# Performance work log

Hardware: AMD Instinct MI355X
Metric: run time of the kernel (lower is better)

The kernel has to match this reference:

```python
import jax, jax.numpy as jnp
import numpy as np

B, T_TEXT, T_MEL = 8, 256, 1024
VOCAB, MEL, H = 256, 80, 512
NH, HD = 8, 64  # MultiheadAttention: 8 heads, head_dim 64


def _linear(x, w, b):
    return x @ w.T + b


def _lstm(x, w_ih, w_hh, b_ih, b_hh, reverse=False):
    # torch LSTM, gate order i,f,g,o; x: [B,T,Din] -> [B,T,H]
    xg = jnp.einsum('bti,gi->btg', x, w_ih) + b_ih  # precompute input contributions
    h0 = jnp.zeros((x.shape[0], w_hh.shape[1]), x.dtype)

    def step(carry, xt):
        h, c = carry
        g = xt + h @ w_hh.T + b_hh
        i, f, gg, o = jnp.split(g, 4, axis=-1)
        c = jax.nn.sigmoid(f) * c + jax.nn.sigmoid(i) * jnp.tanh(gg)
        h = jax.nn.sigmoid(o) * jnp.tanh(c)
        return (h, c), h

    _, hs = jax.lax.scan(step, (h0, h0), jnp.swapaxes(xg, 0, 1), reverse=reverse)
    return jnp.swapaxes(hs, 0, 1)


def _length_regulate(enc, durations, max_len):
    # Vectorized equivalent of the nested python loop: token j owns output
    # positions [cum[j-1], cum[j]); padded positions are zero, mask True=pad.
    dur = jnp.round(durations).astype(jnp.int32)
    cum = jnp.cumsum(dur, axis=1)                              # [B,T_text]
    pos = jnp.arange(max_len)                                  # [max_len]
    idx = jax.vmap(lambda c: jnp.searchsorted(c, pos, side='right'))(cum)
    pad_mask = pos[None, :] >= cum[:, -1:]                     # True = padded
    idx = jnp.minimum(idx, enc.shape[1] - 1)
    exp = jnp.take_along_axis(enc, idx[..., None], axis=1)     # [B,max_len,H]
    exp = exp * (~pad_mask)[..., None].astype(enc.dtype)
    return exp, pad_mask


def setup_inputs() -> dict:
    key = jax.random.key(0)
    ks = jax.random.split(key, 40)

    def rn(k, shape, scale=0.02):
        return jax.random.normal(k, shape, jnp.float32) * scale

    inp = {}
    inp['phoneme_indices'] = jax.random.randint(ks[0], (B, T_TEXT), 0, VOCAB)
    inp['mel_specs'] = jax.random.normal(ks[1], (B, T_MEL, MEL), jnp.float32)
    inp['phoneme_durations'] = jax.random.randint(ks[2], (B, T_TEXT), 0, 8).astype(jnp.float32)
    # parameters
    inp['emb'] = rn(ks[3], (VOCAB, H), 1.0)
    inp['enc_w_ih_f'] = rn(ks[4], (4 * H, H))
    inp['enc_w_hh_f'] = rn(ks[5], (4 * H, H))
    inp['enc_b_ih_f'] = rn(ks[6], (4 * H,))
    inp['enc_b_hh_f'] = rn(ks[7], (4 * H,))
    inp['enc_w_ih_b'] = rn(ks[8], (4 * H, H))
    inp['enc_w_hh_b'] = rn(ks[9], (4 * H, H))
    inp['enc_b_ih_b'] = rn(ks[10], (4 * H,))
    inp['enc_b_hh_b'] = rn(ks[11], (4 * H,))
    inp['proj_w'] = rn(ks[12], (H, 2 * H))
    inp['proj_b'] = rn(ks[13], (H,))
    inp['dur_w1'] = rn(ks[14], (H, H))
    inp['dur_b1'] = rn(ks[15], (H,))
    inp['dur_w2'] = rn(ks[16], (H // 2, H))
    inp['dur_b2'] = rn(ks[17], (H // 2,))
    inp['dur_w3'] = rn(ks[18], (1, H // 2))
    inp['dur_b3'] = rn(ks[19], (1,))
    inp['mel_in_w'] = rn(ks[20], (H, MEL))
    inp['mel_in_b'] = rn(ks[21], (H,))
    inp['attn_in_w'] = rn(ks[22], (3 * H, H))
    inp['attn_in_b'] = rn(ks[23], (3 * H,))
    inp['attn_out_w'] = rn(ks[24], (H, H))
    inp['attn_out_b'] = rn(ks[25], (H,))
    inp['dec_w_ih'] = rn(ks[26], (4 * H, 2 * H))
    inp['dec_w_hh'] = rn(ks[27], (4 * H, H))
    inp['dec_b_ih'] = rn(ks[28], (4 * H,))
    inp['dec_b_hh'] = rn(ks[29], (4 * H,))
    inp['mel_out_w'] = rn(ks[30], (MEL, H))
    inp['mel_out_b'] = rn(ks[31], (MEL,))
    return inp


def reference(phoneme_indices, mel_specs, phoneme_durations, emb,
              enc_w_ih_f, enc_w_hh_f, enc_b_ih_f, enc_b_hh_f,
              enc_w_ih_b, enc_w_hh_b, enc_b_ih_b, enc_b_hh_b,
              proj_w, proj_b, dur_w1, dur_b1, dur_w2, dur_b2, dur_w3, dur_b3,
              mel_in_w, mel_in_b, attn_in_w, attn_in_b, attn_out_w, attn_out_b,
              dec_w_ih, dec_w_hh, dec_b_ih, dec_b_hh, mel_out_w, mel_out_b):
    b = phoneme_indices.shape[0]
    # encode_text (dropout = identity in eval)
    x = emb[phoneme_indices]                                   # [B,T_text,H]
    hf = _lstm(x, enc_w_ih_f, enc_w_hh_f, enc_b_ih_f, enc_b_hh_f)
    hb = _lstm(x, enc_w_ih_b, enc_w_hh_b, enc_b_ih_b, enc_b_hh_b, reverse=True)
    enc = _linear(jnp.concatenate([hf, hb], axis=-1), proj_w, proj_b)
    # duration predictor
    h1 = jax.nn.relu(_linear(enc, dur_w1, dur_b1))
    h2 = jax.nn.relu(_linear(h1, dur_w2, dur_b2))
    log_dur = _linear(h2, dur_w3, dur_b3)[..., 0]              # [B,T_text]
    # length regulation to mel length
    exp, pad_mask = _length_regulate(enc, phoneme_durations, mel_specs.shape[1])
    # teacher-forced decoder: queries depend only on shifted mel targets,
    # so the per-timestep attention loop == one batched MHA over all steps.
    mel_in = jnp.concatenate([jnp.zeros_like(mel_specs[:, :1]), mel_specs[:, :-1]], axis=1)
    q_in = _linear(mel_in, mel_in_w, mel_in_b)                 # [B,T_mel,H]
    wq, wk, wv = jnp.split(attn_in_w, 3, axis=0)
    bq, bk, bv = jnp.split(attn_in_b, 3, axis=0)
    q = _linear(q_in, wq, bq).reshape(b, -1, NH, HD)
    k = _linear(exp, wk, bk).reshape(b, -1, NH, HD)
    v = _linear(exp, wv, bv).reshape(b, -1, NH, HD)
    scores = jnp.einsum('bqhd,bkhd->bhqk', q, k) / np.sqrt(HD).astype(np.float32)
    scores = jnp.where(pad_mask[:, None, None, :], jnp.asarray(-1e9, scores.dtype), scores)
    attn = jax.nn.softmax(scores, axis=-1)
    ctx = jnp.einsum('bhqk,bkhd->bqhd', attn, v).reshape(b, -1, H)
    attended = _linear(ctx, attn_out_w, attn_out_b)
    # decoder LSTM over full sequence (the only true recurrence)
    dec_in = jnp.concatenate([q_in, attended], axis=-1)        # [B,T_mel,2H]
    dec_out = _lstm(dec_in, dec_w_ih, dec_w_hh, dec_b_ih, dec_b_hh)
    mel_pred = _linear(dec_out, mel_out_w, mel_out_b)          # [B,T_mel,MEL]
    return mel_pred, log_dur
```

## Files before the change

kernel.cpp:

```cpp
#include <hip/hip_runtime.h>
#include <hip/hip_bf16.h>


typedef unsigned short u16;
typedef unsigned int u32;
typedef unsigned long long u64;
typedef short short8 __attribute__((ext_vector_type(8)));
typedef float float4_ __attribute__((ext_vector_type(4)));

__device__ __forceinline__ u16 f2b16(float f) {
  u32 u = __float_as_uint(f);
  u = (u + 0x7FFF + ((u >> 16) & 1)) >> 16;
  return (u16)u;
}
__device__ __forceinline__ float b2f(u16 h) { return __uint_as_float((u32)h << 16); }
__device__ __forceinline__ float sigm(float x) { return 1.f / (1.f + __expf(-x)); }
__device__ __forceinline__ float tanh_(float x) { return 2.f / (1.f + __expf(-2.f * x)) - 1.f; }

__global__ void f2b_k(const float* __restrict__ s, u16* __restrict__ d, int n) {
  for (int i = blockIdx.x * 256 + threadIdx.x; i < n; i += gridDim.x * 256) d[i] = f2b16(s[i]);
}
__global__ void permconv_k(const float* __restrict__ s, u16* __restrict__ d, int K) {
  int row = blockIdx.x; int u = row >> 2, G = row & 3;
  const float* sr = s + (long)(G * 512 + u) * K;
  u16* dr = d + (long)row * K;
  for (int c = threadIdx.x; c < K; c += 256) dr[c] = f2b16(sr[c]);
}
__global__ void biascomb_k(const float* __restrict__ bih, const float* __restrict__ bhh,
                           float* __restrict__ out) {
  int r = blockIdx.x * 256 + threadIdx.x;
  int u = r >> 2, G = r & 3;
  out[r] = bih[G * 512 + u] + bhh[G * 512 + u];
}
__global__ void melinw_k(const float* __restrict__ s, u16* __restrict__ d) {
  int row = blockIdx.x, c = threadIdx.x;
  d[row * 128 + c] = (c < 80) ? f2b16(s[row * 80 + c]) : (u16)0;
}
__global__ void meloutw_k(const float* __restrict__ s, u16* __restrict__ d) {
  int row = blockIdx.x;
  for (int c = threadIdx.x; c < 512; c += 256)
    d[row * 512 + c] = (row < 80) ? f2b16(s[row * 512 + c]) : (u16)0;
}
__global__ void biaspad_k(const float* __restrict__ s, float* __restrict__ d) {
  int t = threadIdx.x;
  d[t] = (t < 80) ? s[t] : 0.f;
}
__global__ void embed_k(const int* __restrict__ pid, const float* __restrict__ emb,
                        u16* __restrict__ x) {
  int t = blockIdx.x, b = blockIdx.y;
  int row = pid[b * 256 + t];
  const float* e = emb + (long)row * 512;
  u16* xr = x + ((long)b * 256 + t) * 512;
  xr[threadIdx.x] = f2b16(e[threadIdx.x]);
  xr[threadIdx.x + 256] = f2b16(e[threadIdx.x + 256]);
}
__global__ void melin_k(const float* __restrict__ mel, u16* __restrict__ out) {
  int t = blockIdx.x, b = blockIdx.y, c = threadIdx.x;
  float v = (c < 80 && t > 0) ? mel[((long)b * 1024 + (t - 1)) * 80 + c] : 0.f;
  out[((long)b * 1024 + t) * 128 + c] = f2b16(v);
}
__global__ void cumsum_k(const float* __restrict__ dur, int* __restrict__ cum,
                         int* __restrict__ Lb) {
  int b = blockIdx.x, t = threadIdx.x;
  __shared__ int sd[256];
  sd[t] = __float2int_rn(dur[b * 256 + t]);
  __syncthreads();
  for (int o = 1; o < 256; o <<= 1) {
    int v = (t >= o) ? sd[t - o] : 0;
    __syncthreads();
    sd[t] += v;
    __syncthreads();
  }
  cum[b * 256 + t] = sd[t];
  if (t == 255) Lb[b] = min(sd[255], 1024);
}
__global__ void gather_k(const int* __restrict__ cum, const u16* __restrict__ enc,
                         u16* __restrict__ exp_) {
  int pos = blockIdx.x, b = blockIdx.y;
  const int* cb = cum + b * 256;
  int last = cb[255];
  u32 val = 0;
  if (pos < last) {
    int lo = 0, hi = 255;
    while (lo < hi) { int mid = (lo + hi) >> 1; if (cb[mid] > pos) hi = mid; else lo = mid + 1; }
    val = ((const u32*)(enc + ((long)b * 256 + lo) * 512))[threadIdx.x];
  }
  ((u32*)(exp_ + ((long)b * 1024 + pos) * 512))[threadIdx.x] = val;
}
__global__ void softmax_k(const float* __restrict__ sbuf, u16* __restrict__ P,
                          const int* __restrict__ Lb) {
  int qp = blockIdx.x, b = blockIdx.y;
  const float* s = sbuf + ((long)b * 1024 + qp) * 1024;
  u16* p = P + ((long)b * 1024 + qp) * 1024;
  int L = Lb[b];
  __shared__ float red[256];
  int tid = threadIdx.x;
  float m = -1e30f;
  for (int i = tid; i < L; i += 256) m = fmaxf(m, s[i]);
  red[tid] = m; __syncthreads();
  for (int o = 128; o > 0; o >>= 1) { if (tid < o) red[tid] = fmaxf(red[tid], red[tid + o]); __syncthreads(); }
  float mx = red[0];
  __syncthreads();
  float sm = 0.f;
  for (int i = tid; i < L; i += 256) sm += __expf(s[i] - mx);
  red[tid] = sm; __syncthreads();
  for (int o = 128; o > 0; o >>= 1) { if (tid < o) red[tid] += red[tid + o]; __syncthreads(); }
  float inv = 1.f / red[0];
  for (int i = tid; i < 1024; i += 256) {
    float v = (i < L) ? __expf(s[i] - mx) * inv : 0.f;
    p[i] = f2b16(v);
  }
}
__global__ void dur3_k(const u16* __restrict__ h2, const float* __restrict__ w3,
                       const float* __restrict__ b3, float* __restrict__ out) {
  int row = blockIdx.x * 4 + (threadIdx.x >> 6);
  int l = threadIdx.x & 63;
  const u16* hr = h2 + (long)row * 256;
  float s = 0.f;
  for (int i = 0; i < 4; i++) { int c = l * 4 + i; s += b2f(hr[c]) * w3[c]; }
  for (int o = 32; o > 0; o >>= 1) s += __shfl_down(s, o);
  if (l == 0) out[row] = s + b3[0];
}

__global__ __launch_bounds__(256) void gemm_bt(
    const u16* __restrict__ A, const u16* __restrict__ A2, int ksplit, int lda, int lda2, long sA,
    const u16* __restrict__ B, int ldb, long sB, void* __restrict__ Cv, int ldc, long sC,
    const float* __restrict__ bias, float alpha, int N, int K, int flags) {
  __shared__ u16 As[128 * 72];
  __shared__ u16 Bs[128 * 72];
  int z = blockIdx.z;
  const u16* Ab = A + (long)z * sA;
  const u16* A2b = A2 ? (A2 + (long)z * sA) : (const u16*)0;
  const u16* Bb = B + (long)z * sB;
  int m0 = blockIdx.x * 128, n0 = blockIdx.y * 128;
  int tid = threadIdx.x, wave = tid >> 6, lane = tid & 63;
  int wm = wave & 1, wn = wave >> 1;
  int nl = lane & 15, kb = (lane >> 4) * 8, ml = (lane >> 4) * 4;
  float4_ acc[4][4];
  for (int i = 0; i < 4; i++)
    for (int j = 0; j < 4; j++) { acc[i][j][0] = 0; acc[i][j][1] = 0; acc[i][j][2] = 0; acc[i][j][3] = 0; }
  int rr = tid >> 3, cc = (tid & 7) * 8;
  for (int k0 = 0; k0 < K; k0 += 64) {
    int gk = k0 + cc;
#pragma unroll
    for (int i = 0; i < 4; i++) {
      int row = rr + i * 32;
      const u16* sa = (gk < ksplit) ? (Ab + (long)(m0 + row) * lda + gk)
                                    : (A2b + (long)(m0 + row) * lda2 + (gk - ksplit));
      *(short8*)&As[row * 72 + cc] = *(const short8*)sa;
      *(short8*)&Bs[row * 72 + cc] = *(const short8*)(Bb + (long)(n0 + row) * ldb + gk);
    }
    __syncthreads();
#pragma unroll
    for (int kk = 0; kk < 64; kk += 32) {
      short8 af[4], bfr[4];
#pragma unroll
      for (int i = 0; i < 4; i++) af[i] = *(const short8*)&As[(wm * 64 + i * 16 + nl) * 72 + kk + kb];
#pragma unroll
      for (int i = 0; i < 4; i++) bfr[i] = *(const short8*)&Bs[(wn * 64 + i * 16 + nl) * 72 + kk + kb];
#pragma unroll
      for (int mi = 0; mi < 4; mi++)
#pragma unroll
        for (int ni = 0; ni < 4; ni++)
          acc[mi][ni] = __builtin_amdgcn_mfma_f32_16x16x32_bf16(af[mi], bfr[ni], acc[mi][ni], 0, 0, 0);
    }
    __syncthreads();
  }
  for (int ni = 0; ni < 4; ni++) {
    int n = n0 + wn * 64 + ni * 16 + nl;
    if (n >= N) continue;
    float bv = bias ? bias[n] : 0.f;
    for (int mi = 0; mi < 4; mi++) {
#pragma unroll
      for (int r = 0; r < 4; r++) {
        int m = m0 + wm * 64 + mi * 16 + ml + r;
        float v = acc[mi][ni][r] * alpha + bv;
        if (flags & 2) v = fmaxf(v, 0.f);
        long idx = (flags & 4) ? ((long)n * ldc + m) : ((long)m * ldc + n);
        if (flags & 1) ((u16*)Cv)[z * sC + idx] = f2b16(v);
        else ((float*)Cv)[z * sC + idx] = v;
      }
    }
  }
}


__global__ __launch_bounds__(256) void enc_rec_k(
    const float* __restrict__ xg_f, const float* __restrict__ xg_b,
    const u16* __restrict__ whh_f, const u16* __restrict__ whh_b,
    u16* __restrict__ hcat, u64* __restrict__ hglob) {
  int dir = blockIdx.x >> 5, wg = blockIdx.x & 31;
  int tid = threadIdx.x, wave = tid >> 6, lane = tid & 63;
  int nl = lane & 15, kb = (lane >> 4) * 8, ml = (lane >> 4) * 4;
  int nt = wg * 4 + wave;
  const float* xg = dir ? xg_b : xg_f;
  const u16* whh = dir ? whh_b : whh_f;
  u64* hg = hglob + dir * 4096;
  __shared__ u16 h_s[2][16 * 520];
  __shared__ float gbuf[4][16][17];
  __shared__ float c_s[4][4][8];
  short8 warr[16];
  {
    const u16* wr = whh + (long)(wg * 64 + wave * 16 + nl) * 512 + kb;
#pragma unroll
    for (int kc = 0; kc < 16; kc++) warr[kc] = *(const short8*)(wr + kc * 32);
  }
  if (lane < 32) c_s[wave][lane & 3][lane >> 2] = 0.f;
  __syncthreads();
  float nxt[4];
  {
    int t0 = dir ? 255 : 0;
#pragma unroll
    for (int r = 0; r < 4; r++) {
      int m = ml + r;
      nxt[r] = (m < 8) ? xg[((long)m * 256 + t0) * 2048 + nt * 16 + nl] : 0.f;
    }
  }
  int prow = tid >> 5, c32 = tid & 31;
  for (int s = 0; s < 256; ++s) {
    int t = dir ? 255 - s : s;
    int pb = s & 1;
    float cur0 = nxt[0], cur1 = nxt[1], cur2 = nxt[2], cur3 = nxt[3];
    if (s > 0) {
      const u64* hp = hg + (long)pb * 2048 + prow * 256 + c32 * 2;
      u64 a[8];
      u32 tg = (u32)s;
      for (;;) {
#pragma unroll
        for (int j = 0; j < 4; j++) {
          a[2 * j] = __hip_atomic_load(hp + j * 64, __ATOMIC_RELAXED, __HIP_MEMORY_SCOPE_AGENT);
          a[2 * j + 1] =
              __hip_atomic_load(hp + j * 64 + 1, __ATOMIC_RELAXED, __HIP_MEMORY_SCOPE_AGENT);
        }
        u32 bad = 0;
#pragma unroll
        for (int i = 0; i < 8; i++) bad |= ((u32)(a[i] >> 32) ^ tg);
        if (!bad) break;
      }
      u64* dp = (u64*)(h_s[pb] + prow * 520);
#pragma unroll
      for (int j = 0; j < 4; j++)
        dp[c32 + j * 32] = (a[2 * j] & 0xffffffffull) | (a[2 * j + 1] << 32);
    }
    __builtin_amdgcn_sched_barrier(0);
    if (s + 1 < 256) {
      int tn = dir ? 255 - (s + 1) : (s + 1);
#pragma unroll
      for (int r = 0; r < 4; r++) {
        int m = ml + r;
        nxt[r] = (m < 8) ? xg[((long)m * 256 + tn) * 2048 + nt * 16 + nl] : 0.f;
      }
    }
    __syncthreads();
    float4_ ac0, ac1, ac2, ac3;
    ac0[0] = cur0; ac0[1] = cur1; ac0[2] = cur2; ac0[3] = cur3;
    ac1[0] = 0; ac1[1] = 0; ac1[2] = 0; ac1[3] = 0;
    ac2 = ac1; ac3 = ac1;
    if (s > 0) {
      const u16* hrow = h_s[pb] + nl * 520 + kb;
#pragma unroll
      for (int kc = 0; kc < 16; kc += 4) {
        ac0 = __builtin_amdgcn_mfma_f32_16x16x32_bf16(
            *(const short8*)(hrow + (kc + 0) * 32), warr[kc + 0], ac0, 0, 0, 0);
        ac1 = __builtin_amdgcn_mfma_f32_16x16x32_bf16(
            *(const short8*)(hrow + (kc + 1) * 32), warr[kc + 1], ac1, 0, 0, 0);
        ac2 = __builtin_amdgcn_mfma_f32_16x16x32_bf16(
            *(const short8*)(hrow + (kc + 2) * 32), warr[kc + 2], ac2, 0, 0, 0);
        ac3 = __builtin_amdgcn_mfma_f32_16x16x32_bf16(
            *(const short8*)(hrow + (kc + 3) * 32), warr[kc + 3], ac3, 0, 0, 0);
      }
    }
    float4_ acc = (ac0 + ac1) + (ac2 + ac3);
    gbuf[wave][nl][ml + 0] = acc[0];
    gbuf[wave][nl][ml + 1] = acc[1];
    gbuf[wave][nl][ml + 2] = acc[2];
    gbuf[wave][nl][ml + 3] = acc[3];
    if (lane < 32) {
      int ul = lane & 3, b = lane >> 2;
      float gi = gbuf[wave][ul * 4 + 0][b];
      float gf = gbuf[wave][ul * 4 + 1][b];
      float gg = gbuf[wave][ul * 4 + 2][b];
      float go = gbuf[wave][ul * 4 + 3][b];
      float c = c_s[wave][ul][b];
      c = sigm(gf) * c + sigm(gi) * tanh_(gg);
      float h = sigm(go) * tanh_(c);
      c_s[wave][ul][b] = c;
      int u = nt * 4 + ul;
      u16 hb2 = f2b16(h);
      u32 partner = (u32)__shfl_down((int)hb2, 1);
      if ((ul & 1) == 0) {
        u32 pair = (u32)hb2 | (partner << 16);
        *(u32*)&hcat[((long)b * 256 + t) * 1024 + dir * 512 + u] = pair;
        u64 word = (u64)pair | ((u64)(u32)(s + 1) << 32);
        __hip_atomic_store(hg + (long)((s + 1) & 1) * 2048 + b * 256 + (u >> 1), word,
                           __ATOMIC_RELAXED, __HIP_MEMORY_SCOPE_AGENT);
      }
    }
  }
}

__global__ __launch_bounds__(256) void dec_rec_k(
    const float* __restrict__ xg, const u16* __restrict__ whh,
    u16* __restrict__ dec_out, u64* __restrict__ hglob) {
  int wg = blockIdx.x;
  int tid = threadIdx.x, wave = tid >> 6, lane = tid & 63;
  int nl = lane & 15, kb = (lane >> 4) * 8, ml = (lane >> 4) * 4;
  int nt = wg * 4 + wave;
  __shared__ u16 h_s[2][16 * 520];
  __shared__ float gbuf[4][16][17];
  __shared__ float c_s[4][4][8];
  short8 warr[16];
  {
    const u16* wr = whh + (long)(wg * 64 + wave * 16 + nl) * 512 + kb;
#pragma unroll
    for (int kc = 0; kc < 16; kc++) warr[kc] = *(const short8*)(wr + kc * 32);
  }
  if (lane < 32) c_s[wave][lane & 3][lane >> 2] = 0.f;
  __syncthreads();
  float nxt[4];
#pragma unroll
  for (int r = 0; r < 4; r++) {
    int m = ml + r;
    nxt[r] = (m < 8) ? xg[((long)m * 1024 + 0) * 2048 + nt * 16 + nl] : 0.f;
  }
  int prow = tid >> 5, c32 = tid & 31;
  for (int s = 0; s < 1024; ++s) {
    int pb = s & 1;
    float cur0 = nxt[0], cur1 = nxt[1], cur2 = nxt[2], cur3 = nxt[3];
    if (s > 0) {
      const u64* hp = hglob + (long)pb * 2048 + prow * 256 + c32 * 2;
      u64 a[8];
      u32 tg = (u32)s;
      for (;;) {
#pragma unroll
        for (int j = 0; j < 4; j++) {
          a[2 * j] = __hip_atomic_load(hp + j * 64, __ATOMIC_RELAXED, __HIP_MEMORY_SCOPE_AGENT);
          a[2 * j + 1] =
              __hip_atomic_load(hp + j * 64 + 1, __ATOMIC_RELAXED, __HIP_MEMORY_SCOPE_AGENT);
        }
        u32 bad = 0;
#pragma unroll
        for (int i = 0; i < 8; i++) bad |= ((u32)(a[i] >> 32) ^ tg);
        if (!bad) break;
      }
      u64* dp = (u64*)(h_s[pb] + prow * 520);
#pragma unroll
      for (int j = 0; j < 4; j++)
        dp[c32 + j * 32] = (a[2 * j] & 0xffffffffull) | (a[2 * j + 1] << 32);
    }
    __builtin_amdgcn_sched_barrier(0);
    if (s + 1 < 1024) {
#pragma unroll
      for (int r = 0; r < 4; r++) {
        int m = ml + r;
        nxt[r] = (m < 8) ? xg[((long)m * 1024 + (s + 1)) * 2048 + nt * 16 + nl] : 0.f;
      }
    }
    __syncthreads();
    float4_ ac0, ac1, ac2, ac3;
    ac0[0] = cur0; ac0[1] = cur1; ac0[2] = cur2; ac0[3] = cur3;
    ac1[0] = 0; ac1[1] = 0; ac1[2] = 0; ac1[3] = 0;
    ac2 = ac1; ac3 = ac1;
    if (s > 0) {
      const u16* hrow = h_s[pb] + nl * 520 + kb;
#pragma unroll
      for (int kc = 0; kc < 16; kc += 4) {
        ac0 = __builtin_amdgcn_mfma_f32_16x16x32_bf16(
            *(const short8*)(hrow + (kc + 0) * 32), warr[kc + 0], ac0, 0, 0, 0);
        ac1 = __builtin_amdgcn_mfma_f32_16x16x32_bf16(
            *(const short8*)(hrow + (kc + 1) * 32), warr[kc + 1], ac1, 0, 0, 0);
        ac2 = __builtin_amdgcn_mfma_f32_16x16x32_bf16(
            *(const short8*)(hrow + (kc + 2) * 32), warr[kc + 2], ac2, 0, 0, 0);
        ac3 = __builtin_amdgcn_mfma_f32_16x16x32_bf16(
            *(const short8*)(hrow + (kc + 3) * 32), warr[kc + 3], ac3, 0, 0, 0);
      }
    }
    float4_ acc = (ac0 + ac1) + (ac2 + ac3);
    gbuf[wave][nl][ml + 0] = acc[0];
    gbuf[wave][nl][ml + 1] = acc[1];
    gbuf[wave][nl][ml + 2] = acc[2];
    gbuf[wave][nl][ml + 3] = acc[3];
    if (lane < 32) {
      int ul = lane & 3, b = lane >> 2;
      float gi = gbuf[wave][ul * 4 + 0][b];
      float gf = gbuf[wave][ul * 4 + 1][b];
      float gg = gbuf[wave][ul * 4 + 2][b];
      float go = gbuf[wave][ul * 4 + 3][b];
      float c = c_s[wave][ul][b];
      c = sigm(gf) * c + sigm(gi) * tanh_(gg);
      float h = sigm(go) * tanh_(c);
      c_s[wave][ul][b] = c;
      int u = nt * 4 + ul;
      u16 hb2 = f2b16(h);
      u32 partner = (u32)__shfl_down((int)hb2, 1);
      if ((ul & 1) == 0) {
        u32 pair = (u32)hb2 | (partner << 16);
        *(u32*)&dec_out[((long)b * 1024 + s) * 512 + u] = pair;
        u64 word = (u64)pair | ((u64)(u32)(s + 1) << 32);
        __hip_atomic_store(hglob + (long)((s + 1) & 1) * 2048 + b * 256 + (u >> 1), word,
                           __ATOMIC_RELAXED, __HIP_MEMORY_SCOPE_AGENT);
      }
    }
  }
}

extern "C" void kernel_launch(void* const* d_in, const int* in_sizes, int n_in,
                              void* d_out, int out_size, void* d_ws, size_t ws_size,
                              hipStream_t stream) {
  (void)in_sizes; (void)n_in; (void)out_size; (void)ws_size;
  const int* pid = (const int*)d_in[0];
  const float* mel = (const float*)d_in[1];
  const float* dur = (const float*)d_in[2];
  const float* emb = (const float*)d_in[3];
  const float* e_ihf = (const float*)d_in[4];
  const float* e_hhf = (const float*)d_in[5];
  const float* e_bihf = (const float*)d_in[6];
  const float* e_bhhf = (const float*)d_in[7];
  const float* e_ihb = (const float*)d_in[8];
  const float* e_hhb = (const float*)d_in[9];
  const float* e_bihb = (const float*)d_in[10];
  const float* e_bhhb = (const float*)d_in[11];
  const float* proj_w = (const float*)d_in[12];
  const float* proj_b = (const float*)d_in[13];
  const float* dw1 = (const float*)d_in[14];
  const float* db1 = (const float*)d_in[15];
  const float* dw2 = (const float*)d_in[16];
  const float* db2 = (const float*)d_in[17];
  const float* dw3 = (const float*)d_in[18];
  const float* db3 = (const float*)d_in[19];
  const float* miw = (const float*)d_in[20];
  const float* mib = (const float*)d_in[21];
  const float* aiw = (const float*)d_in[22];
  const float* aib = (const float*)d_in[23];
  const float* aow = (const float*)d_in[24];
  const float* aob = (const float*)d_in[25];
  const float* d_ih = (const float*)d_in[26];
  const float* d_hh = (const float*)d_in[27];
  const float* d_bih = (const float*)d_in[28];
  const float* d_bhh = (const float*)d_in[29];
  const float* mow = (const float*)d_in[30];
  const float* mob = (const float*)d_in[31];
  float* out = (float*)d_out;

  char* W = (char*)d_ws;
  constexpr size_t o_xgf = 0;
  constexpr size_t o_xgb = o_xgf + 16777216;
  constexpr size_t o_sbuf = o_xgb + 16777216;
  constexpr size_t o_decxg = o_xgf;
  constexpr size_t o_pool = o_sbuf + 33554432;
  constexpr size_t o_x = o_pool;
  constexpr size_t o_hcat = o_x + 2097152;
  constexpr size_t o_dh1 = o_hcat + 4194304;
  constexpr size_t o_dh2 = o_dh1 + 2097152;
  constexpr size_t o_melin = o_dh2 + 1048576;
  constexpr size_t o_att = o_pool;
  constexpr size_t o_enc = o_melin + 2097152;
  constexpr size_t o_exp = o_enc + 2097152;
  constexpr size_t o_ctx = o_exp;
  constexpr size_t o_qin = o_exp + 8388608;
  constexpr size_t o_q = o_qin + 8388608;
  constexpr size_t o_decout = o_q;
  constexpr size_t o_k = o_q + 8388608;
  constexpr size_t o_vt = o_k + 8388608;
  constexpr size_t o_p = o_vt + 8519680;
  constexpr size_t o_w0 = o_p + 16777216;
  constexpr size_t o_w_eihf = o_w0;
  constexpr size_t o_w_eihb = o_w_eihf + 2097152;
  constexpr size_t o_w_ehhf = o_w_eihb + 2097152;
  constexpr size_t o_w_ehhb = o_w_ehhf + 2097152;
  constexpr size_t o_w_dih = o_w_ehhb + 2097152;
  constexpr size_t o_w_dhh = o_w_dih + 4194304;
  constexpr size_t o_w_proj = o_w_dhh + 2097152;
  constexpr size_t o_w_d1 = o_w_proj + 1048576;
  constexpr size_t o_w_d2 = o_w_d1 + 524288;
  constexpr size_t o_w_ai = o_w_d2 + 262144;
  constexpr size_t o_w_ao = o_w_ai + 1572864;
  constexpr size_t o_w_mi = o_w_ao + 524288;
  constexpr size_t o_w_mo = o_w_mi + 131072;
  constexpr size_t o_bc_ef = o_w_mo + 131072;
  constexpr size_t o_bc_eb = o_bc_ef + 8192;
  constexpr size_t o_bc_d = o_bc_eb + 8192;
  constexpr size_t o_b_mo = o_bc_d + 8192;
  constexpr size_t o_cum = o_b_mo + 512;
  constexpr size_t o_lb = o_cum + 8192;
  constexpr size_t o_hge = o_lb + 256;
  constexpr size_t o_hgd = o_hge + 65536;

  hipMemsetAsync(W + o_hge, 0, 98304, stream);

  f2b_k<<<512, 256, 0, stream>>>(proj_w, (u16*)(W + o_w_proj), 512 * 1024);
  f2b_k<<<512, 256, 0, stream>>>(dw1, (u16*)(W + o_w_d1), 512 * 512);
  f2b_k<<<256, 256, 0, stream>>>(dw2, (u16*)(W + o_w_d2), 256 * 512);
  f2b_k<<<512, 256, 0, stream>>>(aiw, (u16*)(W + o_w_ai), 1536 * 512);
  f2b_k<<<512, 256, 0, stream>>>(aow, (u16*)(W + o_w_ao), 512 * 512);
  permconv_k<<<2048, 256, 0, stream>>>(e_ihf, (u16*)(W + o_w_eihf), 512);
  permconv_k<<<2048, 256, 0, stream>>>(e_ihb, (u16*)(W + o_w_eihb), 512);
  permconv_k<<<2048, 256, 0, stream>>>(e_hhf, (u16*)(W + o_w_ehhf), 512);
  permconv_k<<<2048, 256, 0, stream>>>(e_hhb, (u16*)(W + o_w_ehhb), 512);
  permconv_k<<<2048, 256, 0, stream>>>(d_ih, (u16*)(W + o_w_dih), 1024);
  permconv_k<<<2048, 256, 0, stream>>>(d_hh, (u16*)(W + o_w_dhh), 512);
  biascomb_k<<<8, 256, 0, stream>>>(e_bihf, e_bhhf, (float*)(W + o_bc_ef));
  biascomb_k<<<8, 256, 0, stream>>>(e_bihb, e_bhhb, (float*)(W + o_bc_eb));
  biascomb_k<<<8, 256, 0, stream>>>(d_bih, d_bhh, (float*)(W + o_bc_d));
  melinw_k<<<512, 128, 0, stream>>>(miw, (u16*)(W + o_w_mi));
  meloutw_k<<<128, 256, 0, stream>>>(mow, (u16*)(W + o_w_mo));
  biaspad_k<<<1, 128, 0, stream>>>(mob, (float*)(W + o_b_mo));

  auto gemm = [&](size_t oA, size_t oA2, int ksplit, int lda, int lda2, long sA, size_t oB,
                  int ldb, long sB, void* C, int ldc, long sC, const float* bias, float alpha,
                  int M, int N, int K, int flags, int batch) {
    dim3 g(M / 128, (N + 127) / 128, batch);
    gemm_bt<<<g, 256, 0, stream>>>((const u16*)(W + oA),
                                   oA2 ? (const u16*)(W + oA2) : (const u16*)0, ksplit, lda, lda2,
                                   sA, (const u16*)(W + oB), ldb, sB, C, ldc, sC, bias, alpha, N,
                                   K, flags);
  };

  embed_k<<<dim3(256, 8), 256, 0, stream>>>(pid, emb, (u16*)(W + o_x));
  gemm(o_x, 0, 512, 512, 0, 0, o_w_eihf, 512, 0, W + o_xgf, 2048, 0,
       (const float*)(W + o_bc_ef), 1.f, 2048, 2048, 512, 0, 1);
  gemm(o_x, 0, 512, 512, 0, 0, o_w_eihb, 512, 0, W + o_xgb, 2048, 0,
       (const float*)(W + o_bc_eb), 1.f, 2048, 2048, 512, 0, 1);
  enc_rec_k<<<64, 256, 0, stream>>>((const float*)(W + o_xgf), (const float*)(W + o_xgb),
                                    (const u16*)(W + o_w_ehhf), (const u16*)(W + o_w_ehhb),
                                    (u16*)(W + o_hcat), (u64*)(W + o_hge));
  gemm(o_hcat, 0, 1024, 1024, 0, 0, o_w_proj, 1024, 0, W + o_enc, 512, 0, proj_b, 1.f, 2048, 512,
       1024, 1, 1);
  gemm(o_enc, 0, 512, 512, 0, 0, o_w_d1, 512, 0, W + o_dh1, 512, 0, db1, 1.f, 2048, 512, 512, 3, 1);
  gemm(o_dh1, 0, 512, 512, 0, 0, o_w_d2, 512, 0, W + o_dh2, 256, 0, db2, 1.f, 2048, 256, 512, 3, 1);
  dur3_k<<<512, 256, 0, stream>>>((const u16*)(W + o_dh2), dw3, db3, out + 655360);
  cumsum_k<<<8, 256, 0, stream>>>(dur, (int*)(W + o_cum), (int*)(W + o_lb));
  gather_k<<<dim3(1024, 8), 256, 0, stream>>>((const int*)(W + o_cum), (const u16*)(W + o_enc),
                                              (u16*)(W + o_exp));
  melin_k<<<dim3(1024, 8), 128, 0, stream>>>(mel, (u16*)(W + o_melin));
  gemm(o_melin, 0, 128, 128, 0, 0, o_w_mi, 128, 0, W + o_qin, 512, 0, mib, 1.f, 8192, 512, 128, 1, 1);
  gemm(o_qin, 0, 512, 512, 0, 0, o_w_ai, 512, 0, W + o_q, 512, 0, aib, 1.f, 8192, 512, 512, 1, 1);
  gemm(o_exp, 0, 512, 512, 0, 0, o_w_ai + (size_t)512 * 512 * 2, 512, 0, W + o_k, 512, 0,
       aib + 512, 1.f, 8192, 512, 512, 1, 1);
  gemm(o_exp, 0, 512, 512, 0, 524288, o_w_ai + (size_t)1024 * 512 * 2, 512, 0, W + o_vt, 1024,
       524288, aib + 1024, 1.f, 1024, 512, 512, 5, 8);
  for (int h = 0; h < 8; h++) {
    gemm(o_q + (size_t)h * 128, 0, 64, 512, 0, 524288, o_k + (size_t)h * 128, 512, 524288,
         W + o_sbuf, 1024, 1048576, (const float*)0, 0.125f, 1024, 1024, 64, 0, 8);
    softmax_k<<<dim3(1024, 8), 256, 0, stream>>>((const float*)(W + o_sbuf), (u16*)(W + o_p),
                                                 (const int*)(W + o_lb));
    gemm(o_p, 0, 1024, 1024, 0, 1048576, o_vt + (size_t)h * 64 * 1024 * 2, 1024, 524288,
         (u16*)(W + o_ctx) + h * 64, 512, 524288, (const float*)0, 1.f, 1024, 64, 1024, 1, 8);
  }
  gemm(o_ctx, 0, 512, 512, 0, 0, o_w_ao, 512, 0, W + o_att, 512, 0, aob, 1.f, 8192, 512, 512, 1, 1);
  gemm(o_qin, o_att, 512, 512, 512, 0, o_w_dih, 1024, 0, W + o_decxg, 2048, 0,
       (const float*)(W + o_bc_d), 1.f, 8192, 2048, 1024, 0, 1);
  dec_rec_k<<<32, 256, 0, stream>>>((const float*)(W + o_decxg), (const u16*)(W + o_w_dhh),
                                    (u16*)(W + o_decout), (u64*)(W + o_hgd));
  gemm(o_decout, 0, 512, 512, 0, 0, o_w_mo, 512, 0, d_out, 80, 0, (const float*)(W + o_b_mo), 1.f,
       8192, 80, 512, 0, 1);
}
```

Before: 3.158 ms.

## Prefetch next-step hidden-state polls early and skip self-owned slices via local LDS write

In both persistent LSTM recurrence kernels, the global atomic loads for the next step's hidden state are issued right after the MFMA accumulation. The spin loop then re-polls only the slices whose tag is stale, so part of the cross-workgroup handoff latency overlaps with the gate math. Each workgroup also writes its own freshly computed h pair straight into LDS and skips polling the slice it owns, which removes one global round trip for local data. The early loads will often see stale tags and need extra polls. The ownership mask and LDS indexing must match the producer layout, or stale data will be read.

After: 3.593 ms. 13.8% more time.

```diff
diff --git a/kernel.cpp b/kernel.cpp
--- a/kernel.cpp
+++ b/kernel.cpp
@@ -217,30 +217,39 @@
     }
   }
   int prow = tid >> 5, c32 = tid & 31;
+  u32 ownm = 0;
+#pragma unroll
+  for (int j = 0; j < 4; j++)
+    if (((j * 64 + c32 * 2) >> 3) == wg) ownm |= 1u << j;
+  u64 a[8];
   for (int s = 0; s < 256; ++s) {
     int t = dir ? 255 - s : s;
     int pb = s & 1;
     float cur0 = nxt[0], cur1 = nxt[1], cur2 = nxt[2], cur3 = nxt[3];
     if (s > 0) {
       const u64* hp = hg + (long)pb * 2048 + prow * 256 + c32 * 2;
-      u64 a[8];
       u32 tg = (u32)s;
       for (;;) {
-#pragma unroll
-        for (int j = 0; j < 4; j++) {
-          a[2 * j] = __hip_atomic_load(hp + j * 64, __ATOMIC_RELAXED, __HIP_MEMORY_SCOPE_AGENT);
-          a[2 * j + 1] =
-              __hip_atomic_load(hp + j * 64 + 1, __ATOMIC_RELAXED, __HIP_MEMORY_SCOPE_AGENT);
-        }
         u32 bad = 0;
 #pragma unroll
-        for (int i = 0; i < 8; i++) bad |= ((u32)(a[i] >> 32) ^ tg);
+        for (int j = 0; j < 4; j++)
+          if (!((ownm >> j) & 1))
+            bad |= ((u32)(a[2 * j] >> 32) ^ tg) | ((u32)(a[2 * j + 1] >> 32) ^ tg);
         if (!bad) break;
+#pragma unroll
+        for (int j = 0; j < 4; j++)
+          if (!((ownm >> j) & 1) &&
+              ((((u32)(a[2 * j] >> 32)) ^ tg) | (((u32)(a[2 * j + 1] >> 32)) ^ tg))) {
+            a[2 * j] = __hip_atomic_load(hp + j * 64, __ATOMIC_RELAXED, __HIP_MEMORY_SCOPE_AGENT);
+            a[2 * j + 1] =
+                __hip_atomic_load(hp + j * 64 + 1, __ATOMIC_RELAXED, __HIP_MEMORY_SCOPE_AGENT);
+          }
       }
       u64* dp = (u64*)(h_s[pb] + prow * 520);
 #pragma unroll
       for (int j = 0; j < 4; j++)
-        dp[c32 + j * 32] = (a[2 * j] & 0xffffffffull) | (a[2 * j + 1] << 32);
+        if (!((ownm >> j) & 1))
+          dp[c32 + j * 32] = (a[2 * j] & 0xffffffffull) | (a[2 * j + 1] << 32);
     }
     __builtin_amdgcn_sched_barrier(0);
     if (s + 1 < 256) {
@@ -271,6 +280,17 @@
       }
     }
     float4_ acc = (ac0 + ac1) + (ac2 + ac3);
+    if (s + 1 < 256) {
+      const u64* hp2 = hg + (long)((s + 1) & 1) * 2048 + prow * 256 + c32 * 2;
+#pragma unroll
+      for (int j = 0; j < 4; j++)
+        if (!((ownm >> j) & 1)) {
+          a[2 * j] = __hip_atomic_load(hp2 + j * 64, __ATOMIC_RELAXED, __HIP_MEMORY_SCOPE_AGENT);
+          a[2 * j + 1] =
+              __hip_atomic_load(hp2 + j * 64 + 1, __ATOMIC_RELAXED, __HIP_MEMORY_SCOPE_AGENT);
+        }
+    }
+    __builtin_amdgcn_sched_barrier(0);
     gbuf[wave][nl][ml + 0] = acc[0];
     gbuf[wave][nl][ml + 1] = acc[1];
     gbuf[wave][nl][ml + 2] = acc[2];
@@ -294,6 +314,7 @@
         u64 word = (u64)pair | ((u64)(u32)(s + 1) << 32);
         __hip_atomic_store(hg + (long)((s + 1) & 1) * 2048 + b * 256 + (u >> 1), word,
                            __ATOMIC_RELAXED, __HIP_MEMORY_SCOPE_AGENT);
+        ((u32*)&h_s[(s + 1) & 1][0])[b * 260 + (u >> 1)] = pair;
       }
     }
   }
@@ -324,29 +345,38 @@
     nxt[r] = (m < 8) ? xg[((long)m * 1024 + 0) * 2048 + nt * 16 + nl] : 0.f;
   }
   int prow = tid >> 5, c32 = tid & 31;
+  u32 ownm = 0;
+#pragma unroll
+  for (int j = 0; j < 4; j++)
+    if (((j * 64 + c32 * 2) >> 3) == wg) ownm |= 1u << j;
+  u64 a[8];
   for (int s = 0; s < 1024; ++s) {
     int pb = s & 1;
     float cur0 = nxt[0], cur1 = nxt[1], cur2 = nxt[2], cur3 = nxt[3];
     if (s > 0) {
       const u64* hp = hglob + (long)pb * 2048 + prow * 256 + c32 * 2;
-      u64 a[8];
       u32 tg = (u32)s;
       for (;;) {
-#pragma unroll
-        for (int j = 0; j < 4; j++) {
-          a[2 * j] = __hip_atomic_load(hp + j * 64, __ATOMIC_RELAXED, __HIP_MEMORY_SCOPE_AGENT);
-          a[2 * j + 1] =
-              __hip_atomic_load(hp + j * 64 + 1, __ATOMIC_RELAXED, __HIP_MEMORY_SCOPE_AGENT);
-        }
         u32 bad = 0;
 #pragma unroll
-        for (int i = 0; i < 8; i++) bad |= ((u32)(a[i] >> 32) ^ tg);
+        for (int j = 0; j < 4; j++)
+          if (!((ownm >> j) & 1))
+            bad |= ((u32)(a[2 * j] >> 32) ^ tg) | ((u32)(a[2 * j + 1] >> 32) ^ tg);
         if (!bad) break;
+#pragma unroll
+        for (int j = 0; j < 4; j++)
+          if (!((ownm >> j) & 1) &&
+              ((((u32)(a[2 * j] >> 32)) ^ tg) | (((u32)(a[2 * j + 1] >> 32)) ^ tg))) {
+            a[2 * j] = __hip_atomic_load(hp + j * 64, __ATOMIC_RELAXED, __HIP_MEMORY_SCOPE_AGENT);
+            a[2 * j + 1] =
+                __hip_atomic_load(hp + j * 64 + 1, __ATOMIC_RELAXED, __HIP_MEMORY_SCOPE_AGENT);
+          }
       }
       u64* dp = (u64*)(h_s[pb] + prow * 520);
 #pragma unroll
       for (int j = 0; j < 4; j++)
-        dp[c32 + j * 32] = (a[2 * j] & 0xffffffffull) | (a[2 * j + 1] << 32);
+        if (!((ownm >> j) & 1))
+          dp[c32 + j * 32] = (a[2 * j] & 0xffffffffull) | (a[2 * j + 1] << 32);
     }
     __builtin_amdgcn_sched_barrier(0);
     if (s + 1 < 1024) {
@@ -376,6 +406,17 @@
       }
     }
     float4_ acc = (ac0 + ac1) + (ac2 + ac3);
+    if (s + 1 < 1024) {
+      const u64* hp2 = hglob + (long)((s + 1) & 1) * 2048 + prow * 256 + c32 * 2;
+#pragma unroll
+      for (int j = 0; j < 4; j++)
+        if (!((ownm >> j) & 1)) {
+          a[2 * j] = __hip_atomic_load(hp2 + j * 64, __ATOMIC_RELAXED, __HIP_MEMORY_SCOPE_AGENT);
+          a[2 * j + 1] =
+              __hip_atomic_load(hp2 + j * 64 + 1, __ATOMIC_RELAXED, __HIP_MEMORY_SCOPE_AGENT);
+        }
+    }
+    __builtin_amdgcn_sched_barrier(0);
     gbuf[wave][nl][ml + 0] = acc[0];
     gbuf[wave][nl][ml + 1] = acc[1];
     gbuf[wave][nl][ml + 2] = acc[2];
@@ -399,6 +440,7 @@
         u64 word = (u64)pair | ((u64)(u32)(s + 1) << 32);
         __hip_atomic_store(hglob + (long)((s + 1) & 1) * 2048 + b * 256 + (u >> 1), word,
                            __ATOMIC_RELAXED, __HIP_MEMORY_SCOPE_AGENT);
+        ((u32*)&h_s[(s + 1) & 1][0])[b * 260 + (u >> 1)] = pair;
       }
     }
   }
```
